# Kernel optimization log

Measured on AMD Instinct MI355X. Metric: run time of the kernel, lower is better.

Reference implementation:

```python
import jax, jax.numpy as jnp
import numpy as np

B = 16384      # batch
D_IN = 512     # layer_channels[0]
D = 1024       # hidden width (layer_channels[1..4])
R = 16         # num_relations
SCALE = 0.02


def setup_inputs() -> dict:
    key = jax.random.key(0)
    ks = jax.random.split(key, 8)
    return {
        "x": jax.random.normal(ks[0], (B, D_IN), dtype=jnp.float32),
        "relations": jax.random.randint(ks[1], (B,), 0, R, dtype=jnp.int32),
        # non-relation dense stack (2 layers)
        "W0": jax.random.normal(ks[2], (D_IN, D), dtype=jnp.float32) * SCALE,
        "b0": jnp.zeros((D,), dtype=jnp.float32),
        "W1": jax.random.normal(ks[3], (D, D), dtype=jnp.float32) * SCALE,
        "b1": jnp.zeros((D,), dtype=jnp.float32),
        # relation-aware layers (3 layers due to the module's range(i, num_layers))
        "RW1": jax.random.normal(ks[4], (R, D, D), dtype=jnp.float32) * SCALE,
        "Rb1": jnp.zeros((R, D), dtype=jnp.float32),
        "RW2": jax.random.normal(ks[5], (R, D, D), dtype=jnp.float32) * SCALE,
        "Rb2": jnp.zeros((R, D), dtype=jnp.float32),
        "RW3": jax.random.normal(ks[6], (R, D, D), dtype=jnp.float32) * SCALE,
        "Rb3": jnp.zeros((R, D), dtype=jnp.float32),
    }


def _relation_linear(h, W, b, relations):
    """Per-sample weight selection: out[n] = h[n] @ W[rel[n]] + b[rel[n]].
    Computed as R masked GEMMs to avoid materializing per-sample [B,D,D] weights.
    """
    out = jnp.zeros((h.shape[0], W.shape[2]), dtype=h.dtype)
    for r in range(W.shape[0]):  # fixed small expert set -> ok to unroll
        mask = (relations == r)[:, None]
        out = out + jnp.where(mask, h @ W[r] + b[r], jnp.zeros((), h.dtype))
    return out


def reference(x, relations, W0, b0, W1, b1, RW1, Rb1, RW2, Rb2, RW3, Rb3):
    # non_relation_pred: Linear -> ReLU -> (dropout=identity), twice
    h = jax.nn.relu(x @ W0 + b0)
    h = jax.nn.relu(h @ W1 + b1)
    # relation layers: relu+dropout between, none after last; bn disabled
    h = jax.nn.relu(_relation_linear(h, RW1, Rb1, relations))
    h = jax.nn.relu(_relation_linear(h, RW2, Rb2, relations))
    h = _relation_linear(h, RW3, Rb3, relations)
    return h
```

## Files before the change

kernel.cpp:

```cpp
#include <hip/hip_runtime.h>
#include <stdint.h>

#define B_ROWS   16384
#define D_IN     512
#define N_DIM    1024
#define NREL     16
#define TM       128
#define TN       128
#define BK       32
#define MAX_TILES 144
#define PADDED_ROWS (MAX_TILES * TM)

typedef __bf16 bf16x8 __attribute__((ext_vector_type(8)));
typedef float  f32x4  __attribute__((ext_vector_type(4)));

__device__ __forceinline__ uint16_t f2bf(float f) {
  union { float f; uint32_t u; } v; v.f = f;
  return (uint16_t)((v.u + 0x7fffu + ((v.u >> 16) & 1u)) >> 16);
}

__device__ __forceinline__ void async_cp16(const uint16_t* g, uint16_t* l) {
  __builtin_amdgcn_global_load_lds(
      (__attribute__((address_space(1))) void*)(g),
      (__attribute__((address_space(3))) void*)(l), 16, 0, 0);
}

__global__ void setup_kernel(const int* __restrict__ rel, int* __restrict__ rowidx,
                             int* __restrict__ texp, int* __restrict__ tval) {
  __shared__ int cnt[NREL], segstart[NREL], cursor[NREL];
  const int t = threadIdx.x;
  if (t < NREL) { cnt[t] = 0; cursor[t] = 0; }
  __syncthreads();
  for (int i = t; i < B_ROWS; i += 256) atomicAdd(&cnt[rel[i]], 1);
  __syncthreads();
  if (t == 0) {
    int slot = 0, tile = 0;
    for (int r = 0; r < NREL; r++) {
      segstart[r] = slot;
      const int c = cnt[r];
      const int nt = (c + TM - 1) / TM;
      for (int k = 0; k < nt; k++) {
        texp[tile + k] = r;
        const int rem = c - k * TM;
        tval[tile + k] = rem < TM ? rem : TM;
      }
      tile += nt; slot += nt * TM;
    }
    for (; tile < MAX_TILES; tile++) { texp[tile] = 0; tval[tile] = 0; }
  }
  __syncthreads();
  for (int i = t; i < PADDED_ROWS; i += 256) rowidx[i] = 0;
  __syncthreads();
  for (int i = t; i < B_ROWS; i += 256) {
    const int r = rel[i];
    const int p = atomicAdd(&cursor[r], 1);
    rowidx[segstart[r] + p] = i;
  }
}

__global__ void conv_x_kernel(const float* __restrict__ in, uint16_t* __restrict__ out, int n4) {
  const int i = blockIdx.x * blockDim.x + threadIdx.x;
  if (i < n4) {
    const float4 v = ((const float4*)in)[i];
    uint2 o;
    o.x = (uint32_t)f2bf(v.x) | ((uint32_t)f2bf(v.y) << 16);
    o.y = (uint32_t)f2bf(v.z) | ((uint32_t)f2bf(v.w) << 16);
    ((uint2*)out)[i] = o;
  }
}

__global__ __launch_bounds__(256)
void transpose_conv_kernel(const float* __restrict__ W, uint16_t* __restrict__ Wt,
                           int K, int N) {
  __shared__ uint32_t t32[64][33];
  const size_t mat = (size_t)K * N;
  const float*    Wp  = W  + mat * blockIdx.z;
  uint16_t*       Wtp = Wt + mat * blockIdx.z;
  const int n0 = blockIdx.x * 64, k0 = blockIdx.y * 64;
  const int tx = threadIdx.x & 15;
  const int ty = threadIdx.x >> 4;
  #pragma unroll
  for (int rb = 0; rb < 2; rb++) {
    const int kp = rb * 16 + ty;
    const int k  = k0 + kp * 2;
    const float4 r0 = *(const float4*)&Wp[(size_t)k * N + n0 + tx * 4];
    const float4 r1 = *(const float4*)&Wp[(size_t)(k + 1) * N + n0 + tx * 4];
    t32[tx * 4 + 0][kp] = (uint32_t)f2bf(r0.x) | ((uint32_t)f2bf(r1.x) << 16);
    t32[tx * 4 + 1][kp] = (uint32_t)f2bf(r0.y) | ((uint32_t)f2bf(r1.y) << 16);
    t32[tx * 4 + 2][kp] = (uint32_t)f2bf(r0.z) | ((uint32_t)f2bf(r1.z) << 16);
    t32[tx * 4 + 3][kp] = (uint32_t)f2bf(r0.w) | ((uint32_t)f2bf(r1.w) << 16);
  }
  __syncthreads();
  #pragma unroll
  for (int rb = 0; rb < 4; rb++) {
    const int nl = rb * 16 + ty;
    uint2 v; v.x = t32[nl][2 * tx]; v.y = t32[nl][2 * tx + 1];
    *(uint2*)&Wtp[(size_t)(n0 + nl) * K + k0 + tx * 4] = v;
  }
}

template<bool GATHER, bool EXPERT, bool RELU, bool SCATTER>
__global__ __launch_bounds__(256)
void gemm_kernel(const uint16_t* __restrict__ A, const uint16_t* __restrict__ W,
                 const float* __restrict__ bias, void* __restrict__ outp,
                 const int* __restrict__ rowidx, const int* __restrict__ texp,
                 const int* __restrict__ tval, int K) {
  __shared__ uint16_t sA[TM * BK];
  __shared__ uint16_t sB[TN * BK];

  const int tid = threadIdx.x;
  const int w = tid >> 6, l = tid & 63;

  const int lin = blockIdx.x;
  const int xcd = lin & 7;
  const int j   = lin >> 3;
  const int mpx = gridDim.x >> 6;
  const int my  = xcd * mpx + (j >> 3);
  const int nx  = j & 7;
  const int m0 = my * TM;
  const int n0 = nx * TN;

  int e = 0, valid = TM;
  if (EXPERT) {
    e = texp[my];
    valid = tval[my];
    if (valid == 0) return;
  }

  const int lrow16 = l >> 2;
  const int row0   = 16 * w + lrow16;
  const int sel    = (row0 ^ (row0 >> 2)) & 3;
  const int koff   = ((l & 3) ^ sel) * 8;
  int ar0 = m0 + row0, ar1 = m0 + 64 + row0;
  if (GATHER) { ar0 = rowidx[ar0]; ar1 = rowidx[ar1]; }
  const uint16_t* srcA0 = A + (size_t)ar0 * K + koff;
  const uint16_t* srcA1 = A + (size_t)ar1 * K + koff;
  const uint16_t* Wb    = W + (size_t)e * N_DIM * K;
  const uint16_t* srcB0 = Wb + (size_t)(n0 + row0) * K + koff;
  const uint16_t* srcB1 = Wb + (size_t)(n0 + 64 + row0) * K + koff;
  uint16_t* ldsA0 = &sA[w * 512 + l * 8];
  uint16_t* ldsA1 = &sA[2048 + w * 512 + l * 8];
  uint16_t* ldsB0 = &sB[w * 512 + l * 8];
  uint16_t* ldsB1 = &sB[2048 + w * 512 + l * 8];

  const int wm = w >> 1, wn = w & 1;
  const int q = l >> 4, r16 = l & 15;
  const int selr = (r16 ^ (r16 >> 2)) & 3;

  f32x4 acc[4][4];
  #pragma unroll
  for (int i = 0; i < 4; i++)
    #pragma unroll
    for (int jj = 0; jj < 4; jj++) {
      f32x4 z = {0.f, 0.f, 0.f, 0.f};
      acc[i][jj] = z;
    }

  for (int k0 = 0; k0 < K; k0 += BK) {
    async_cp16(srcA0 + k0, ldsA0);
    async_cp16(srcA1 + k0, ldsA1);
    async_cp16(srcB0 + k0, ldsB0);
    async_cp16(srcB1 + k0, ldsB1);
    __syncthreads();
    bf16x8 af[4], bf[4];
    const int cq = (q ^ selr) * 8;
    #pragma unroll
    for (int i = 0; i < 4; i++) {
      af[i] = *(const bf16x8*)(&sA[(wm * 64 + i * 16 + r16) * BK + cq]);
      bf[i] = *(const bf16x8*)(&sB[(wn * 64 + i * 16 + r16) * BK + cq]);
    }
    #pragma unroll
    for (int i = 0; i < 4; i++)
      #pragma unroll
      for (int jj = 0; jj < 4; jj++)
        acc[i][jj] = __builtin_amdgcn_mfma_f32_16x16x32_bf16(af[i], bf[jj], acc[i][jj], 0, 0, 0);
    __syncthreads();
  }

  float bj[4];
  #pragma unroll
  for (int jj = 0; jj < 4; jj++)
    bj[jj] = bias[(size_t)e * N_DIM + n0 + wn * 64 + jj * 16 + r16];

  #pragma unroll
  for (int i = 0; i < 4; i++) {
    #pragma unroll
    for (int r = 0; r < 4; r++) {
      const int rl = wm * 64 + i * 16 + q * 4 + r;
      if (SCATTER) {
        if (rl < valid) {
          const int orow = rowidx[m0 + rl];
          float* o = (float*)outp + (size_t)orow * N_DIM + n0 + wn * 64 + r16;
          #pragma unroll
          for (int jj = 0; jj < 4; jj++) {
            float v = acc[i][jj][r] + bj[jj];
            if (RELU) v = fmaxf(v, 0.f);
            o[jj * 16] = v;
          }
        }
      } else {
        uint16_t* o = (uint16_t*)outp + (size_t)(m0 + rl) * N_DIM + n0 + wn * 64 + r16;
        #pragma unroll
        for (int jj = 0; jj < 4; jj++) {
          float v = acc[i][jj][r] + bj[jj];
          if (RELU) v = fmaxf(v, 0.f);
          o[jj * 16] = f2bf(v);
        }
      }
    }
  }
}

extern "C" void kernel_launch(void* const* d_in, const int* in_sizes, int n_in,
                              void* d_out, int out_size, void* d_ws, size_t ws_size,
                              hipStream_t stream) {
  const float* x   = (const float*)d_in[0];
  const int*   rel = (const int*)d_in[1];
  const float* W0  = (const float*)d_in[2];
  const float* b0  = (const float*)d_in[3];
  const float* W1  = (const float*)d_in[4];
  const float* b1  = (const float*)d_in[5];
  const float* RW1 = (const float*)d_in[6];
  const float* Rb1 = (const float*)d_in[7];
  const float* RW2 = (const float*)d_in[8];
  const float* Rb2 = (const float*)d_in[9];
  const float* RW3 = (const float*)d_in[10];
  const float* Rb3 = (const float*)d_in[11];
  float* out = (float*)d_out;

  char* ws = (char*)d_ws;
  uint16_t* xb = (uint16_t*)(ws);
  uint16_t* wt = (uint16_t*)(ws + (size_t)(16u << 20));
  uint16_t* ha = (uint16_t*)(ws + (size_t)(48u << 20));
  uint16_t* hb = (uint16_t*)(ws + (size_t)(84u << 20));
  int* rowidx = (int*)(ws + (size_t)(120u << 20));
  int* texp   = rowidx + PADDED_ROWS;
  int* tval   = texp + MAX_TILES;

  const dim3 blk(256);
  const dim3 gDense(8 * (B_ROWS / TM));
  const dim3 gRel(8 * MAX_TILES);

  setup_kernel<<<dim3(1), blk, 0, stream>>>(rel, rowidx, texp, tval);
  conv_x_kernel<<<dim3((B_ROWS * D_IN) / 4 / 256), blk, 0, stream>>>(x, xb, (B_ROWS * D_IN) / 4);

  transpose_conv_kernel<<<dim3(N_DIM / 64, D_IN / 64, 1), blk, 0, stream>>>(W0, wt, D_IN, N_DIM);
  gemm_kernel<false, false, true, false><<<gDense, blk, 0, stream>>>(
      xb, wt, b0, ha, nullptr, nullptr, nullptr, D_IN);

  transpose_conv_kernel<<<dim3(N_DIM / 64, N_DIM / 64, 1), blk, 0, stream>>>(W1, wt, N_DIM, N_DIM);
  gemm_kernel<false, false, true, false><<<gDense, blk, 0, stream>>>(
      ha, wt, b1, hb, nullptr, nullptr, nullptr, N_DIM);

  transpose_conv_kernel<<<dim3(N_DIM / 64, N_DIM / 64, NREL), blk, 0, stream>>>(RW1, wt, N_DIM, N_DIM);
  gemm_kernel<true, true, true, false><<<gRel, blk, 0, stream>>>(
      hb, wt, Rb1, ha, rowidx, texp, tval, N_DIM);

  transpose_conv_kernel<<<dim3(N_DIM / 64, N_DIM / 64, NREL), blk, 0, stream>>>(RW2, wt, N_DIM, N_DIM);
  gemm_kernel<false, true, true, false><<<gRel, blk, 0, stream>>>(
      ha, wt, Rb2, hb, rowidx, texp, tval, N_DIM);

  transpose_conv_kernel<<<dim3(N_DIM / 64, N_DIM / 64, NREL), blk, 0, stream>>>(RW3, wt, N_DIM, N_DIM);
  gemm_kernel<false, true, false, true><<<gRel, blk, 0, stream>>>(
      hb, wt, Rb3, out, rowidx, texp, tval, N_DIM);

  (void)in_sizes; (void)n_in; (void)out_size; (void)ws_size;
}
```

Measured before the change: 574.2 us.

## Double-buffer LDS tiles in GEMM and widen setup kernel block

The GEMM main loop now uses two LDS buffers per operand. It issues the async global-to-LDS loads for the next K slice before computing on the current one, using explicit vmcnt waits and raw barriers so memory latency can overlap with MFMA work. The single-block setup kernel is launched with 1024 threads instead of 256 to shorten its serial loops. Doubling LDS per block may lower occupancy. Dropping the LDS waitcnt that __syncthreads provided risks ordering hazards.

New measurement: 520.1 us. -9.4%, faster.

```diff
diff --git a/kernel.cpp b/kernel.cpp
--- a/kernel.cpp
+++ b/kernel.cpp
@@ -29,9 +29,10 @@
                              int* __restrict__ texp, int* __restrict__ tval) {
   __shared__ int cnt[NREL], segstart[NREL], cursor[NREL];
   const int t = threadIdx.x;
+  const int nt_ = blockDim.x;
   if (t < NREL) { cnt[t] = 0; cursor[t] = 0; }
   __syncthreads();
-  for (int i = t; i < B_ROWS; i += 256) atomicAdd(&cnt[rel[i]], 1);
+  for (int i = t; i < B_ROWS; i += nt_) atomicAdd(&cnt[rel[i]], 1);
   __syncthreads();
   if (t == 0) {
     int slot = 0, tile = 0;
@@ -49,9 +50,9 @@
     for (; tile < MAX_TILES; tile++) { texp[tile] = 0; tval[tile] = 0; }
   }
   __syncthreads();
-  for (int i = t; i < PADDED_ROWS; i += 256) rowidx[i] = 0;
-  __syncthreads();
-  for (int i = t; i < B_ROWS; i += 256) {
+  for (int i = t; i < PADDED_ROWS; i += nt_) rowidx[i] = 0;
+  __syncthreads();
+  for (int i = t; i < B_ROWS; i += nt_) {
     const int r = rel[i];
     const int p = atomicAdd(&cursor[r], 1);
     rowidx[segstart[r] + p] = i;
@@ -105,8 +106,8 @@
                  const float* __restrict__ bias, void* __restrict__ outp,
                  const int* __restrict__ rowidx, const int* __restrict__ texp,
                  const int* __restrict__ tval, int K) {
-  __shared__ uint16_t sA[TM * BK];
-  __shared__ uint16_t sB[TN * BK];
+  __shared__ uint16_t sA[2][TM * BK];
+  __shared__ uint16_t sB[2][TN * BK];
 
   const int tid = threadIdx.x;
   const int w = tid >> 6, l = tid & 63;
@@ -127,8 +128,7 @@
     if (valid == 0) return;
   }
 
-  const int lrow16 = l >> 2;
-  const int row0   = 16 * w + lrow16;
+  const int row0   = 16 * w + (l >> 2);
   const int sel    = (row0 ^ (row0 >> 2)) & 3;
   const int koff   = ((l & 3) ^ sel) * 8;
   int ar0 = m0 + row0, ar1 = m0 + 64 + row0;
@@ -138,14 +138,15 @@
   const uint16_t* Wb    = W + (size_t)e * N_DIM * K;
   const uint16_t* srcB0 = Wb + (size_t)(n0 + row0) * K + koff;
   const uint16_t* srcB1 = Wb + (size_t)(n0 + 64 + row0) * K + koff;
-  uint16_t* ldsA0 = &sA[w * 512 + l * 8];
-  uint16_t* ldsA1 = &sA[2048 + w * 512 + l * 8];
-  uint16_t* ldsB0 = &sB[w * 512 + l * 8];
-  uint16_t* ldsB1 = &sB[2048 + w * 512 + l * 8];
+  uint16_t* ldsA0 = &sA[0][w * 512 + l * 8];
+  uint16_t* ldsA1 = &sA[0][2048 + w * 512 + l * 8];
+  uint16_t* ldsB0 = &sB[0][w * 512 + l * 8];
+  uint16_t* ldsB1 = &sB[0][2048 + w * 512 + l * 8];
 
   const int wm = w >> 1, wn = w & 1;
   const int q = l >> 4, r16 = l & 15;
   const int selr = (r16 ^ (r16 >> 2)) & 3;
+  const int cq = (q ^ selr) * 8;
 
   f32x4 acc[4][4];
   #pragma unroll
@@ -156,25 +157,41 @@
       acc[i][jj] = z;
     }
 
-  for (int k0 = 0; k0 < K; k0 += BK) {
-    async_cp16(srcA0 + k0, ldsA0);
-    async_cp16(srcA1 + k0, ldsA1);
-    async_cp16(srcB0 + k0, ldsB0);
-    async_cp16(srcB1 + k0, ldsB1);
-    __syncthreads();
+  const int nIter = K / BK;
+
+  async_cp16(srcA0, ldsA0);
+  async_cp16(srcA1, ldsA1);
+  async_cp16(srcB0, ldsB0);
+  async_cp16(srcB1, ldsB1);
+
+  for (int k = 0; k < nIter; k++) {
+    const int cur = k & 1;
+    if (k + 1 < nIter) {
+      const int koff2 = (k + 1) * BK;
+      const int boff  = (cur ^ 1) * 4096;
+      async_cp16(srcA0 + koff2, ldsA0 + boff);
+      async_cp16(srcA1 + koff2, ldsA1 + boff);
+      async_cp16(srcB0 + koff2, ldsB0 + boff);
+      async_cp16(srcB1 + koff2, ldsB1 + boff);
+      asm volatile("s_waitcnt vmcnt(4)" ::: "memory");
+    } else {
+      asm volatile("s_waitcnt vmcnt(0)" ::: "memory");
+    }
+    __builtin_amdgcn_s_barrier();
+
     bf16x8 af[4], bf[4];
-    const int cq = (q ^ selr) * 8;
     #pragma unroll
     for (int i = 0; i < 4; i++) {
-      af[i] = *(const bf16x8*)(&sA[(wm * 64 + i * 16 + r16) * BK + cq]);
-      bf[i] = *(const bf16x8*)(&sB[(wn * 64 + i * 16 + r16) * BK + cq]);
+      af[i] = *(const bf16x8*)(&sA[cur][(wm * 64 + i * 16 + r16) * BK + cq]);
+      bf[i] = *(const bf16x8*)(&sB[cur][(wn * 64 + i * 16 + r16) * BK + cq]);
     }
     #pragma unroll
     for (int i = 0; i < 4; i++)
       #pragma unroll
       for (int jj = 0; jj < 4; jj++)
         acc[i][jj] = __builtin_amdgcn_mfma_f32_16x16x32_bf16(af[i], bf[jj], acc[i][jj], 0, 0, 0);
-    __syncthreads();
+
+    __builtin_amdgcn_s_barrier();
   }
 
   float bj[4];
@@ -241,7 +258,7 @@
   const dim3 gDense(8 * (B_ROWS / TM));
   const dim3 gRel(8 * MAX_TILES);
 
-  setup_kernel<<<dim3(1), blk, 0, stream>>>(rel, rowidx, texp, tval);
+  setup_kernel<<<dim3(1), dim3(1024), 0, stream>>>(rel, rowidx, texp, tval);
   conv_x_kernel<<<dim3((B_ROWS * D_IN) / 4 / 256), blk, 0, stream>>>(x, xb, (B_ROWS * D_IN) / 4);
 
   transpose_conv_kernel<<<dim3(N_DIM / 64, D_IN / 64, 1), blk, 0, stream>>>(W0, wt, D_IN, N_DIM);
```
